# Kernel optimization log

Hardware: AMD Instinct MI355X
Metric: run time of the kernel (lower is better)

The kernel has to match this reference:

```python
import jax, jax.numpy as jnp
import numpy as np

N_USERS = 50000
N_ITEMS = 10000
N_ENTITIES = 40000
N_NODES = N_USERS + N_ITEMS + N_ENTITIES  # 100000
EMB = 64
NNZ = 1600000  # avg degree 16
VIS_DIM = 2048
TXT_DIM = 300


def setup_inputs() -> dict:
    key = jax.random.key(0)
    ks = jax.random.split(key, 16)
    def xn(k, shape, scale=0.05):
        return jax.random.normal(k, shape, dtype=jnp.float32) * scale
    return {
        "adj_row": jax.random.randint(ks[0], (NNZ,), 0, N_NODES, dtype=jnp.int32),
        "adj_col": jax.random.randint(ks[1], (NNZ,), 0, N_NODES, dtype=jnp.int32),
        "adj_val": jax.random.uniform(ks[2], (NNZ,), dtype=jnp.float32) / 16.0,  # ~normalized adj
        "embedding": xn(ks[3], (N_NODES, EMB), 0.1),
        "visual_features": jax.random.normal(ks[4], (N_ITEMS, VIS_DIM), dtype=jnp.float32),
        "text_features": jax.random.normal(ks[5], (N_ITEMS, TXT_DIM), dtype=jnp.float32),
        "Wv1": xn(ks[6], (512, VIS_DIM)), "bv1": jnp.zeros((512,), jnp.float32),
        "Wv2": xn(ks[7], (EMB, 512)),    "bv2": jnp.zeros((EMB,), jnp.float32),
        "Wt1": xn(ks[8], (256, TXT_DIM)), "bt1": jnp.zeros((256,), jnp.float32),
        "Wt2": xn(ks[9], (EMB, 256)),    "bt2": jnp.zeros((EMB,), jnp.float32),
        "Wd": xn(ks[10], (EMB, EMB)),    "bd": jnp.zeros((EMB,), jnp.float32),
        "Wc0": xn(ks[11], (EMB, 2 * EMB)), "bc0": jnp.zeros((EMB,), jnp.float32),
        "Wc1": xn(ks[12], (EMB, 2 * EMB)), "bc1": jnp.zeros((EMB,), jnp.float32),
    }


def _lin(x, W, b):
    return x @ W.T + b


def reference(adj_row, adj_col, adj_val, embedding, visual_features, text_features,
              Wv1, bv1, Wv2, bv2, Wt1, bt1, Wt2, bt2, Wd, bd, Wc0, bc0, Wc1, bc1):
    # multimodal item encoding (eval mode: dropout = identity)
    vis = _lin(jax.nn.relu(_lin(visual_features, Wv1, bv1)), Wv2, bv2)
    vis = _lin(vis, Wd, bd)
    txt = _lin(jax.nn.relu(_lin(text_features, Wt1, bt1)), Wt2, bt2)
    txt = _lin(txt, Wd, bd)
    fused_item = (vis + txt) * 0.5  # [n_items, emb]

    ego = embedding.at[N_USERS:N_USERS + N_ITEMS].set(fused_item)

    all_embs = [ego]
    cur = ego
    for Wc, bc in ((Wc0, bc0), (Wc1, bc1)):
        # SpMM: neighbor[i] = sum_j A[i,j] * cur[j]
        msgs = adj_val[:, None] * cur[adj_col]            # [nnz, emb]
        nb = jax.ops.segment_sum(msgs, adj_row, num_segments=N_NODES)
        cur = _lin(jnp.concatenate([cur, nb], axis=-1), Wc, bc)  # W_concat
        cur = jax.nn.leaky_relu(cur, 0.01)                # F.leaky_relu default slope
        all_embs.append(cur)

    return jnp.concatenate(all_embs, axis=-1)  # [n_nodes, emb*(n_layers+1)]
```

## Files before the change

kernel.cpp:

```cpp
#include <hip/hip_runtime.h>
#include <hip/hip_bf16.h>
#include <cstddef>

#define N_USERS 50000
#define N_ITEMS 10000
#define N_NODES 100000
#define EMB 64
#define NNZ_E 1600000
#define VIS_DIM 2048
#define TXT_DIM 300

typedef short bf16x8 __attribute__((ext_vector_type(8)));
typedef float f32x4  __attribute__((ext_vector_type(4)));

__device__ inline unsigned short f2bf(float x) {
    __hip_bfloat16 h = __float2bfloat16(x);
    return __builtin_bit_cast(unsigned short, h);
}
__device__ inline float bf2f(unsigned short u) {
    unsigned int t = ((unsigned int)u) << 16;
    float f;
    __builtin_memcpy(&f, &t, 4);
    return f;
}

#define GLDW 40

__global__ __launch_bounds__(256, 2) void gemm_bf64(
    const float* __restrict__ A, const float* __restrict__ W,
    const float* __restrict__ bias, float* __restrict__ C,
    int M, int N, int K, int k_per, long long c_plane,
    int act, int add_bias, int n_tiles, int m_tiles, int zsplit)
{
    __shared__ unsigned short Ah[128][GLDW], Al[128][GLDW];
    __shared__ unsigned short Bh[64][GLDW],  Bl[64][GLDW];

    const int wg     = blockIdx.x;
    const int xcd    = wg & 7;
    const int rest   = wg >> 3;
    const int nzc    = n_tiles * zsplit;
    const int nz     = rest % nzc;
    const int mchunk = rest / nzc;
    const int mt     = xcd + (mchunk << 3);
    if (mt >= m_tiles) return;
    const int nt     = nz % n_tiles;
    const int kz     = nz / n_tiles;

    const int t   = threadIdx.x;
    const int w   = t >> 6;
    const int l   = t & 63;
    const int l16 = l & 15;
    const int lq  = l >> 4;
    const int n0  = nt * 64;
    const int m0  = mt * 128;
    const int mh  = w * 32;

    const int kb  = kz * k_per;
    int krem = K - kb; if (krem > k_per) krem = k_per;
    const int kiters = (krem + 31) / 32;
    const int kend = kb + krem;
    float* Cz = C + (long long)kz * c_plane;

    const int rA0 = t >> 2;
    const int rA1 = (t + 256) >> 2;
    const int kc  = t & 3;

    f32x4 acc[2][4] = {};
    float pa[2][8], pw[8];

    auto load_tile = [&](int kt) {
        const int k0 = kb + kt * 32 + kc * 8;
        #pragma unroll
        for (int p = 0; p < 2; p++) {
            int rg = m0 + (p ? rA1 : rA0);
            if (rg >= M) rg = M - 1;
            const float* g = A + (size_t)rg * K + k0;
            if (k0 + 7 < kend) {
                float4 q0 = *(const float4*)g, q1 = *(const float4*)(g + 4);
                pa[p][0]=q0.x; pa[p][1]=q0.y; pa[p][2]=q0.z; pa[p][3]=q0.w;
                pa[p][4]=q1.x; pa[p][5]=q1.y; pa[p][6]=q1.z; pa[p][7]=q1.w;
            } else {
                #pragma unroll
                for (int i = 0; i < 8; i++)
                    pa[p][i] = (k0 + i < kend) ? g[i] : 0.f;
            }
        }
        int ng = n0 + rA0;
        if (ng >= N) ng = N - 1;
        const float* gw = W + (size_t)ng * K + k0;
        if (k0 + 7 < kend) {
            float4 q0 = *(const float4*)gw, q1 = *(const float4*)(gw + 4);
            pw[0]=q0.x; pw[1]=q0.y; pw[2]=q0.z; pw[3]=q0.w;
            pw[4]=q1.x; pw[5]=q1.y; pw[6]=q1.z; pw[7]=q1.w;
        } else {
            #pragma unroll
            for (int i = 0; i < 8; i++)
                pw[i] = (k0 + i < kend) ? gw[i] : 0.f;
        }
    };

    load_tile(0);

    for (int kt = 0; kt < kiters; kt++) {
        #pragma unroll
        for (int p = 0; p < 2; p++) {
            int row = p ? rA1 : rA0;
            bf16x8 hi, lo;
            #pragma unroll
            for (int i = 0; i < 8; i++) {
                unsigned short h = f2bf(pa[p][i]);
                hi[i] = (short)h;
                lo[i] = (short)f2bf(pa[p][i] - bf2f(h));
            }
            *(bf16x8*)&Ah[row][kc * 8] = hi;
            *(bf16x8*)&Al[row][kc * 8] = lo;
        }
        {
            bf16x8 hi, lo;
            #pragma unroll
            for (int i = 0; i < 8; i++) {
                unsigned short h = f2bf(pw[i]);
                hi[i] = (short)h;
                lo[i] = (short)f2bf(pw[i] - bf2f(h));
            }
            *(bf16x8*)&Bh[rA0][kc * 8] = hi;
            *(bf16x8*)&Bl[rA0][kc * 8] = lo;
        }
        __syncthreads();

        if (kt + 1 < kiters) load_tile(kt + 1);

        {
            bf16x8 ah[2], al[2];
            #pragma unroll
            for (int mi = 0; mi < 2; mi++) {
                ah[mi] = *(const bf16x8*)&Ah[mh + mi * 16 + l16][lq * 8];
                al[mi] = *(const bf16x8*)&Al[mh + mi * 16 + l16][lq * 8];
            }
            #pragma unroll
            for (int ni = 0; ni < 4; ni++) {
                bf16x8 bh = *(const bf16x8*)&Bh[ni * 16 + l16][lq * 8];
                bf16x8 bl = *(const bf16x8*)&Bl[ni * 16 + l16][lq * 8];
                #pragma unroll
                for (int mi = 0; mi < 2; mi++) {
                    acc[mi][ni] = __builtin_amdgcn_mfma_f32_16x16x32_bf16(
                        ah[mi], bh, acc[mi][ni], 0, 0, 0);
                    acc[mi][ni] = __builtin_amdgcn_mfma_f32_16x16x32_bf16(
                        ah[mi], bl, acc[mi][ni], 0, 0, 0);
                    acc[mi][ni] = __builtin_amdgcn_mfma_f32_16x16x32_bf16(
                        al[mi], bh, acc[mi][ni], 0, 0, 0);
                }
            }
        }
        __syncthreads();
    }

    #pragma unroll
    for (int ni = 0; ni < 4; ni++) {
        int col = n0 + ni * 16 + l16;
        if (col >= N) continue;
        float b = (add_bias && kz == 0) ? bias[col] : 0.f;
        #pragma unroll
        for (int mi = 0; mi < 2; mi++) {
            #pragma unroll
            for (int r = 0; r < 4; r++) {
                int row = m0 + mh + mi * 16 + lq * 4 + r;
                if (row >= M) continue;
                float v = acc[mi][ni][r] + b;
                if (act) v = fmaxf(v, 0.f);
                Cz[(size_t)row * N + col] = v;
            }
        }
    }
}

__global__ __launch_bounds__(256, 2) void concat_mfma(
    const float* __restrict__ cur, const float* __restrict__ nbuf,
    const float* __restrict__ Wc, const float* __restrict__ bias,
    float* __restrict__ out_cur, float* __restrict__ out_full, int col_off)
{
    __shared__ unsigned short Ah[128][GLDW], Al[128][GLDW];
    __shared__ unsigned short Bh[64][GLDW],  Bl[64][GLDW];

    const int t   = threadIdx.x;
    const int w   = t >> 6;
    const int l   = t & 63;
    const int l16 = l & 15;
    const int lq  = l >> 4;
    const int m0  = blockIdx.x * 128;
    const int mh  = w * 32;

    const int r  = t >> 2;
    const int kc = t & 3;

    f32x4 acc[2][4] = {};

    float pa[2][8], pw[8];

    auto load_tile = [&](int kt) {
        const float* src = (kt < 2) ? cur : nbuf;
        const int kcol = (kt & 1) * 32 + kc * 8;
        #pragma unroll
        for (int p = 0; p < 2; p++) {
            int rg = m0 + r + p * 64;
            if (rg >= N_NODES) rg = N_NODES - 1;
            const float* g = src + (size_t)rg * 64 + kcol;
            float4 q0 = *(const float4*)g, q1 = *(const float4*)(g + 4);
            pa[p][0]=q0.x; pa[p][1]=q0.y; pa[p][2]=q0.z; pa[p][3]=q0.w;
            pa[p][4]=q1.x; pa[p][5]=q1.y; pa[p][6]=q1.z; pa[p][7]=q1.w;
        }
        const float* gw = Wc + (size_t)r * 128 + kt * 32 + kc * 8;
        float4 q0 = *(const float4*)gw, q1 = *(const float4*)(gw + 4);
        pw[0]=q0.x; pw[1]=q0.y; pw[2]=q0.z; pw[3]=q0.w;
        pw[4]=q1.x; pw[5]=q1.y; pw[6]=q1.z; pw[7]=q1.w;
    };

    load_tile(0);

    for (int kt = 0; kt < 4; kt++) {
        #pragma unroll
        for (int p = 0; p < 2; p++) {
            bf16x8 hi, lo;
            #pragma unroll
            for (int i = 0; i < 8; i++) {
                unsigned short h = f2bf(pa[p][i]);
                hi[i] = (short)h;
                lo[i] = (short)f2bf(pa[p][i] - bf2f(h));
            }
            *(bf16x8*)&Ah[r + p * 64][kc * 8] = hi;
            *(bf16x8*)&Al[r + p * 64][kc * 8] = lo;
        }
        {
            bf16x8 hi, lo;
            #pragma unroll
            for (int i = 0; i < 8; i++) {
                unsigned short h = f2bf(pw[i]);
                hi[i] = (short)h;
                lo[i] = (short)f2bf(pw[i] - bf2f(h));
            }
            *(bf16x8*)&Bh[r][kc * 8] = hi;
            *(bf16x8*)&Bl[r][kc * 8] = lo;
        }
        __syncthreads();

        if (kt < 3) load_tile(kt + 1);

        {
            bf16x8 ah[2], al[2];
            #pragma unroll
            for (int mi = 0; mi < 2; mi++) {
                ah[mi] = *(const bf16x8*)&Ah[mh + mi * 16 + l16][lq * 8];
                al[mi] = *(const bf16x8*)&Al[mh + mi * 16 + l16][lq * 8];
            }
            #pragma unroll
            for (int ni = 0; ni < 4; ni++) {
                bf16x8 bh = *(const bf16x8*)&Bh[ni * 16 + l16][lq * 8];
                bf16x8 bl = *(const bf16x8*)&Bl[ni * 16 + l16][lq * 8];
                #pragma unroll
                for (int mi = 0; mi < 2; mi++) {
                    acc[mi][ni] = __builtin_amdgcn_mfma_f32_16x16x32_bf16(
                        ah[mi], bh, acc[mi][ni], 0, 0, 0);
                    acc[mi][ni] = __builtin_amdgcn_mfma_f32_16x16x32_bf16(
                        ah[mi], bl, acc[mi][ni], 0, 0, 0);
                    acc[mi][ni] = __builtin_amdgcn_mfma_f32_16x16x32_bf16(
                        al[mi], bh, acc[mi][ni], 0, 0, 0);
                }
            }
        }
        __syncthreads();
    }

    #pragma unroll
    for (int ni = 0; ni < 4; ni++) {
        int col = ni * 16 + l16;
        float bcol = bias[col];
        #pragma unroll
        for (int mi = 0; mi < 2; mi++) {
            #pragma unroll
            for (int rr = 0; rr < 4; rr++) {
                int row = m0 + mh + mi * 16 + lq * 4 + rr;
                if (row >= N_NODES) continue;
                float v = acc[mi][ni][rr] + bcol;
                v = (v > 0.f) ? v : 0.01f * v;
                if (out_cur) out_cur[(size_t)row * 64 + col] = v;
                out_full[(size_t)row * 192 + col_off + col] = v;
            }
        }
    }
}

__global__ void transp64(const float* __restrict__ W, float* __restrict__ wT, int K)
{
    int i = blockIdx.x * 256 + threadIdx.x;
    if (i >= 64 * K) return;
    int d = i / K, k = i - d * K;
    wT[k * 64 + d] = W[i];
}

__global__ __launch_bounds__(256) void linear64(
    const float* __restrict__ in, const float* __restrict__ in2,
    const float* __restrict__ wT, const float* __restrict__ bias,
    float* __restrict__ out, int M, int K, float in_scale, int add,
    int fuse_relu)
{
    int t  = threadIdx.x;
    int d  = t & 63;
    int w  = t >> 6;
    int m0 = blockIdx.x * 16 + w * 4;
    if (m0 >= M) return;
    int mlast = M - 1;
    int m1 = (m0 + 1 < M) ? m0 + 1 : mlast;
    int m2 = (m0 + 2 < M) ? m0 + 2 : mlast;
    int m3 = (m0 + 3 < M) ? m0 + 3 : mlast;

    const float* x0 = in + (size_t)m0 * K;
    const float* x1 = in + (size_t)m1 * K;
    const float* x2 = in + (size_t)m2 * K;
    const float* x3 = in + (size_t)m3 * K;
    const float* y0 = fuse_relu ? in2 + (size_t)m0 * K : x0;
    const float* y1 = fuse_relu ? in2 + (size_t)m1 * K : x1;
    const float* y2 = fuse_relu ? in2 + (size_t)m2 * K : x2;
    const float* y3 = fuse_relu ? in2 + (size_t)m3 * K : x3;

    float a0 = 0.f, a1 = 0.f, a2 = 0.f, a3 = 0.f;

    for (int k = 0; k < K; k += 8) {
        const float* wp = wT + (size_t)k * 64 + d;
        float w0 = wp[0],   w1 = wp[64],  w2 = wp[128], w3 = wp[192];
        float w4 = wp[256], w5 = wp[320], w6 = wp[384], w7 = wp[448];
        float4 p0 = *(const float4*)(x0 + k), q0 = *(const float4*)(x0 + k + 4);
        float4 p1 = *(const float4*)(x1 + k), q1 = *(const float4*)(x1 + k + 4);
        float4 p2 = *(const float4*)(x2 + k), q2 = *(const float4*)(x2 + k + 4);
        float4 p3 = *(const float4*)(x3 + k), q3 = *(const float4*)(x3 + k + 4);
        if (fuse_relu) {
            float4 r0 = *(const float4*)(y0 + k), s0 = *(const float4*)(y0 + k + 4);
            float4 r1 = *(const float4*)(y1 + k), s1 = *(const float4*)(y1 + k + 4);
            float4 r2 = *(const float4*)(y2 + k), s2 = *(const float4*)(y2 + k + 4);
            float4 r3 = *(const float4*)(y3 + k), s3 = *(const float4*)(y3 + k + 4);
            p0.x=fmaxf(p0.x+r0.x,0.f); p0.y=fmaxf(p0.y+r0.y,0.f);
            p0.z=fmaxf(p0.z+r0.z,0.f); p0.w=fmaxf(p0.w+r0.w,0.f);
            q0.x=fmaxf(q0.x+s0.x,0.f); q0.y=fmaxf(q0.y+s0.y,0.f);
            q0.z=fmaxf(q0.z+s0.z,0.f); q0.w=fmaxf(q0.w+s0.w,0.f);
            p1.x=fmaxf(p1.x+r1.x,0.f); p1.y=fmaxf(p1.y+r1.y,0.f);
            p1.z=fmaxf(p1.z+r1.z,0.f); p1.w=fmaxf(p1.w+r1.w,0.f);
            q1.x=fmaxf(q1.x+s1.x,0.f); q1.y=fmaxf(q1.y+s1.y,0.f);
            q1.z=fmaxf(q1.z+s1.z,0.f); q1.w=fmaxf(q1.w+s1.w,0.f);
            p2.x=fmaxf(p2.x+r2.x,0.f); p2.y=fmaxf(p2.y+r2.y,0.f);
            p2.z=fmaxf(p2.z+r2.z,0.f); p2.w=fmaxf(p2.w+r2.w,0.f);
            q2.x=fmaxf(q2.x+s2.x,0.f); q2.y=fmaxf(q2.y+s2.y,0.f);
            q2.z=fmaxf(q2.z+s2.z,0.f); q2.w=fmaxf(q2.w+s2.w,0.f);
            p3.x=fmaxf(p3.x+r3.x,0.f); p3.y=fmaxf(p3.y+r3.y,0.f);
            p3.z=fmaxf(p3.z+r3.z,0.f); p3.w=fmaxf(p3.w+r3.w,0.f);
            q3.x=fmaxf(q3.x+s3.x,0.f); q3.y=fmaxf(q3.y+s3.y,0.f);
            q3.z=fmaxf(q3.z+s3.z,0.f); q3.w=fmaxf(q3.w+s3.w,0.f);
        }
        a0 += p0.x*w0 + p0.y*w1 + p0.z*w2 + p0.w*w3
            + q0.x*w4 + q0.y*w5 + q0.z*w6 + q0.w*w7;
        a1 += p1.x*w0 + p1.y*w1 + p1.z*w2 + p1.w*w3
            + q1.x*w4 + q1.y*w5 + q1.z*w6 + q1.w*w7;
        a2 += p2.x*w0 + p2.y*w1 + p2.z*w2 + p2.w*w3
            + q2.x*w4 + q2.y*w5 + q2.z*w6 + q2.w*w7;
        a3 += p3.x*w0 + p3.y*w1 + p3.z*w2 + p3.w*w3
            + q3.x*w4 + q3.y*w5 + q3.z*w6 + q3.w*w7;
    }

    float b = bias[d];
    float r0 = a0 * in_scale + b;
    float r1 = a1 * in_scale + b;
    float r2 = a2 * in_scale + b;
    float r3 = a3 * in_scale + b;
    if (add) {
        out[(size_t)m0 * 64 + d] += r0;
        if (m0 + 1 < M) out[(size_t)m1 * 64 + d] += r1;
        if (m0 + 2 < M) out[(size_t)m2 * 64 + d] += r2;
        if (m0 + 3 < M) out[(size_t)m3 * 64 + d] += r3;
    } else {
        out[(size_t)m0 * 64 + d] = r0;
        if (m0 + 1 < M) out[(size_t)m1 * 64 + d] = r1;
        if (m0 + 2 < M) out[(size_t)m2 * 64 + d] = r2;
        if (m0 + 3 < M) out[(size_t)m3 * 64 + d] = r3;
    }
}

__global__ void ego_fill(const float* __restrict__ emb, float* __restrict__ cur0,
                         float* __restrict__ out_full)
{
    int tid = blockIdx.x * 256 + threadIdx.x;
    if (tid >= N_NODES * EMB) return;
    int m = tid >> 6, d = tid & 63;
    float v;
    if (m < N_USERS || m >= N_USERS + N_ITEMS) {
        v = emb[tid];
        cur0[tid] = v;
    } else {
        v = cur0[tid];
    }
    out_full[(size_t)m * 192 + d] = v;
}

__global__ __launch_bounds__(256) void hist_rows(
    const int* __restrict__ row, int* __restrict__ cnt, int nnz)
{
    int e = blockIdx.x * 256 + threadIdx.x;
    if (e >= nnz) return;
    atomicAdd(&cnt[row[e]], 1);
}

__global__ __launch_bounds__(256) void scan1(int* __restrict__ cnt,
                                             int* __restrict__ bsum, int n)
{
    __shared__ int part[256];
    int t = threadIdx.x;
    int base = blockIdx.x * 1024 + t * 4;
    int v0 = 0, v1 = 0, v2 = 0, v3 = 0;
    if (base + 0 < n) v0 = cnt[base + 0];
    if (base + 1 < n) v1 = cnt[base + 1];
    if (base + 2 < n) v2 = cnt[base + 2];
    if (base + 3 < n) v3 = cnt[base + 3];
    int s = v0 + v1 + v2 + v3;
    part[t] = s;
    __syncthreads();
    for (int off = 1; off < 256; off <<= 1) {
        int x = (t >= off) ? part[t - off] : 0;
        __syncthreads();
        part[t] += x;
        __syncthreads();
    }
    int excl = part[t] - s;
    if (t == 255) bsum[blockIdx.x] = part[t];
    if (base + 0 < n) cnt[base + 0] = excl;
    if (base + 1 < n) cnt[base + 1] = excl + v0;
    if (base + 2 < n) cnt[base + 2] = excl + v0 + v1;
    if (base + 3 < n) cnt[base + 3] = excl + v0 + v1 + v2;
}

__global__ void scan2(int* __restrict__ bsum, int nb)
{
    if (threadIdx.x == 0 && blockIdx.x == 0) {
        int acc = 0;
        for (int i = 0; i < nb; i++) { int v = bsum[i]; bsum[i] = acc; acc += v; }
    }
}

__global__ __launch_bounds__(256) void scan3(
    const int* __restrict__ excl, const int* __restrict__ bsum,
    int* __restrict__ row_ptr, int* __restrict__ row_cur, int n, int nnz)
{
    int i = blockIdx.x * 256 + threadIdx.x;
    if (i > n) return;
    if (i == n) { row_ptr[n] = nnz; return; }
    int v = excl[i] + bsum[i >> 10];
    row_ptr[i] = v;
    row_cur[i] = v;
}

__global__ __launch_bounds__(256) void scatter_csr(
    const int* __restrict__ row, const int* __restrict__ col,
    const float* __restrict__ val, int* __restrict__ row_cur,
    int* __restrict__ col_s, float* __restrict__ val_s, int nnz)
{
    int e = blockIdx.x * 256 + threadIdx.x;
    if (e >= nnz) return;
    int r = row[e];
    int p = atomicAdd(&row_cur[r], 1);
    col_s[p] = col[e];
    val_s[p] = val[e];
}

__global__ __launch_bounds__(256) void spmm_gather(
    const int* __restrict__ row_ptr, const int* __restrict__ col_s,
    const float* __restrict__ val_s, const float* __restrict__ cur,
    float* __restrict__ nb)
{
    int t  = threadIdx.x;
    int wv = t >> 6;
    int l  = t & 63;
    int eg = l >> 4;
    int dg = l & 15;
    int m = blockIdx.x * 4 + wv;
    if (m >= N_NODES) return;
    int beg = row_ptr[m], end = row_ptr[m + 1];
    float ax = 0.f, ay = 0.f, az = 0.f, aw = 0.f;
    for (int j = beg + eg; j < end; j += 4) {
        int   c = col_s[j];
        float v = val_s[j];
        float4 cv = *(const float4*)&cur[(size_t)c * 64 + dg * 4];
        ax += v * cv.x; ay += v * cv.y; az += v * cv.z; aw += v * cv.w;
    }
    ax += __shfl_xor(ax, 16, 64); ay += __shfl_xor(ay, 16, 64);
    az += __shfl_xor(az, 16, 64); aw += __shfl_xor(aw, 16, 64);
    ax += __shfl_xor(ax, 32, 64); ay += __shfl_xor(ay, 32, 64);
    az += __shfl_xor(az, 32, 64); aw += __shfl_xor(aw, 32, 64);
    if (eg == 0) {
        float4 r; r.x = ax; r.y = ay; r.z = az; r.w = aw;
        *(float4*)&nb[(size_t)m * 64 + dg * 4] = r;
    }
}

extern "C" void kernel_launch(void* const* d_in, const int* in_sizes, int n_in,
                              void* d_out, int out_size, void* d_ws, size_t ws_size,
                              hipStream_t stream)
{
    const int*   adj_row = (const int*)  d_in[0];
    const int*   adj_col = (const int*)  d_in[1];
    const float* adj_val = (const float*)d_in[2];
    const float* emb     = (const float*)d_in[3];
    const float* visf    = (const float*)d_in[4];
    const float* txtf    = (const float*)d_in[5];
    const float* Wv1 = (const float*)d_in[6];  const float* bv1 = (const float*)d_in[7];
    const float* Wv2 = (const float*)d_in[8];  const float* bv2 = (const float*)d_in[9];
    const float* Wt1 = (const float*)d_in[10]; const float* bt1 = (const float*)d_in[11];
    const float* Wt2 = (const float*)d_in[12]; const float* bt2 = (const float*)d_in[13];
    const float* Wd  = (const float*)d_in[14]; const float* bd  = (const float*)d_in[15];
    const float* Wc0 = (const float*)d_in[16]; const float* bc0 = (const float*)d_in[17];
    const float* Wc1 = (const float*)d_in[18]; const float* bc1 = (const float*)d_in[19];

    float* out = (float*)d_out;
    float* ws  = (float*)d_ws;

    float* H1v  = ws + 0;
    float* H1t  = ws + 5120000;
    float* nb   = ws + 0;
    float* s    = ws + 7680000;
    float* cur0 = ws + 8320000;
    float* cur1 = ws + 14720000;
    float* H1v2 = ws + 14720000;
    float* wv2T = ws + 21120000;
    float* wt2T = wv2T + 32768;
    float* wdT  = wt2T + 16384;
    int*   col_s   = (int*)  (ws + 21200000);
    float* val_s   =          ws + 22800000;
    int*   row_ptr = (int*)  (ws + 24400000);
    int*   row_cur = (int*)  (ws + 24510000);
    int*   cnt     = (int*)  (ws + 24620000);
    int*   bsum    = (int*)  (ws + 24730000);

    const int NBLK = (N_NODES + 1023) / 1024;

    transp64<<<(64 * 512 + 255) / 256, 256, 0, stream>>>(Wv2, wv2T, 512);
    transp64<<<(64 * 256 + 255) / 256, 256, 0, stream>>>(Wt2, wt2T, 256);
    transp64<<<(64 * 64  + 255) / 256, 256, 0, stream>>>(Wd,  wdT,  64);

    hipMemsetAsync(cnt, 0, N_NODES * sizeof(int), stream);
    hist_rows<<<(NNZ_E + 255) / 256, 256, 0, stream>>>(adj_row, cnt, NNZ_E);
    scan1<<<NBLK, 256, 0, stream>>>(cnt, bsum, N_NODES);
    scan2<<<1, 64, 0, stream>>>(bsum, NBLK);
    scan3<<<(N_NODES + 256) / 256, 256, 0, stream>>>(cnt, bsum, row_ptr, row_cur,
                                                     N_NODES, NNZ_E);
    scatter_csr<<<(NNZ_E + 255) / 256, 256, 0, stream>>>(adj_row, adj_col, adj_val,
                                                         row_cur, col_s, val_s, NNZ_E);

    {
        int n_tiles = 8, m_tiles = 79, zsplit = 2;
        int grid = 8 * n_tiles * zsplit * ((m_tiles + 7) / 8);
        gemm_bf64<<<grid, 256, 0, stream>>>(visf, Wv1, bv1, H1v,
                                            N_ITEMS, 512, VIS_DIM,
                                            1024, (long long)14720000, 0, 1,
                                            n_tiles, m_tiles, zsplit);
    }
    {
        int n_tiles = 4, m_tiles = 79, zsplit = 1;
        int grid = 8 * n_tiles * zsplit * ((m_tiles + 7) / 8);
        gemm_bf64<<<grid, 256, 0, stream>>>(txtf, Wt1, bt1, H1t,
                                            N_ITEMS, 256, TXT_DIM,
                                            512, 0, 1, 1,
                                            n_tiles, m_tiles, zsplit);
    }

    linear64<<<(N_ITEMS + 15) / 16, 256, 0, stream>>>(H1v, H1v2, wv2T, bv2, s,
                                                      N_ITEMS, 512, 1.0f, 0, 1);
    linear64<<<(N_ITEMS + 15) / 16, 256, 0, stream>>>(H1t, nullptr, wt2T, bt2, s,
                                                      N_ITEMS, 256, 1.0f, 1, 0);
    linear64<<<(N_ITEMS + 15) / 16, 256, 0, stream>>>(s, nullptr, wdT, bd,
                                                      cur0 + (size_t)N_USERS * 64,
                                                      N_ITEMS, 64, 0.5f, 0, 0);

    ego_fill<<<(N_NODES * EMB + 255) / 256, 256, 0, stream>>>(emb, cur0, out);

    spmm_gather<<<(N_NODES + 3) / 4, 256, 0, stream>>>(row_ptr, col_s, val_s, cur0, nb);
    concat_mfma<<<(N_NODES + 127) / 128, 256, 0, stream>>>(cur0, nb, Wc0, bc0, cur1, out, 64);

    spmm_gather<<<(N_NODES + 3) / 4, 256, 0, stream>>>(row_ptr, col_s, val_s, cur1, nb);
    concat_mfma<<<(N_NODES + 127) / 128, 256, 0, stream>>>(cur1, nb, Wc1, bc1, nullptr, out, 128);
}
```

Before: 819.2 us.

## Pre-split weights into bf16 hi/lo MFMA fragments and load B from global

Adds a prepass kernel that splits each weight matrix into bf16 high/low parts, stored in an MFMA-fragment-tiled layout. The GEMM and concat kernels then read B fragments directly from global/L2 instead of converting per tile and staging through LDS. This removes the repeated weight splitting and the B shared-memory traffic, and raises the occupancy hint to 4 blocks. In exchange it adds extra launches and puts uncoalesced-ish global loads on the critical path of the MFMA loop.

```diff
diff --git a/kernel.cpp b/kernel.cpp
--- a/kernel.cpp
+++ b/kernel.cpp
@@ -26,14 +26,37 @@
 
 #define GLDW 40
 
-__global__ __launch_bounds__(256, 2) void gemm_bf64(
-    const float* __restrict__ A, const float* __restrict__ W,
+__global__ __launch_bounds__(256) void wsplit_frag(
+    const float* __restrict__ W, unsigned short* __restrict__ Wh,
+    unsigned short* __restrict__ Wl, int N, int K, int Kp)
+{
+    int idx = blockIdx.x * 256 + threadIdx.x;
+    int ncell = Kp >> 3;
+    if (idx >= N * ncell) return;
+    int n = idx / ncell, kcell = idx - n * ncell;
+    int k0 = kcell * 8;
+    bf16x8 hi, lo;
+    #pragma unroll
+    for (int i = 0; i < 8; i++) {
+        float v = (k0 + i < K) ? W[(size_t)n * K + k0 + i] : 0.f;
+        unsigned short h = f2bf(v);
+        hi[i] = (short)h;
+        lo[i] = (short)f2bf(v - bf2f(h));
+    }
+    size_t off = ((size_t)(n >> 4) * ncell + kcell) * 128 + (size_t)(n & 15) * 8;
+    *(bf16x8*)(Wh + off) = hi;
+    *(bf16x8*)(Wl + off) = lo;
+}
+
+__global__ __launch_bounds__(256, 4) void gemm_bf64(
+    const float* __restrict__ A,
+    const unsigned short* __restrict__ Wh_f,
+    const unsigned short* __restrict__ Wl_f,
     const float* __restrict__ bias, float* __restrict__ C,
-    int M, int N, int K, int k_per, long long c_plane,
+    int M, int N, int K, int Kp, int k_per, long long c_plane,
     int act, int add_bias, int n_tiles, int m_tiles, int zsplit)
 {
     __shared__ unsigned short Ah[128][GLDW], Al[128][GLDW];
-    __shared__ unsigned short Bh[64][GLDW],  Bl[64][GLDW];
 
     const int wg     = blockIdx.x;
     const int xcd    = wg & 7;
@@ -61,14 +84,16 @@
     const int kend = kb + krem;
     float* Cz = C + (long long)kz * c_plane;
 
+    const int ncell = Kp >> 3;
+
     const int rA0 = t >> 2;
     const int rA1 = (t + 256) >> 2;
     const int kc  = t & 3;
 
     f32x4 acc[2][4] = {};
-    float pa[2][8], pw[8];
-
-    auto load_tile = [&](int kt) {
+    float pa[2][8];
+
+    auto load_tileA = [&](int kt) {
         const int k0 = kb + kt * 32 + kc * 8;
         #pragma unroll
         for (int p = 0; p < 2; p++) {
@@ -85,21 +110,9 @@
                     pa[p][i] = (k0 + i < kend) ? g[i] : 0.f;
             }
         }
-        int ng = n0 + rA0;
-        if (ng >= N) ng = N - 1;
-        const float* gw = W + (size_t)ng * K + k0;
-        if (k0 + 7 < kend) {
-            float4 q0 = *(const float4*)gw, q1 = *(const float4*)(gw + 4);
-            pw[0]=q0.x; pw[1]=q0.y; pw[2]=q0.z; pw[3]=q0.w;
-            pw[4]=q1.x; pw[5]=q1.y; pw[6]=q1.z; pw[7]=q1.w;
-        } else {
-            #pragma unroll
-            for (int i = 0; i < 8; i++)
-                pw[i] = (k0 + i < kend) ? gw[i] : 0.f;
-        }
     };
 
-    load_tile(0);
+    load_tileA(0);
 
     for (int kt = 0; kt < kiters; kt++) {
         #pragma unroll
@@ -115,20 +128,21 @@
             *(bf16x8*)&Ah[row][kc * 8] = hi;
             *(bf16x8*)&Al[row][kc * 8] = lo;
         }
+        __syncthreads();
+
+        bf16x8 bh[4], bl[4];
         {
-            bf16x8 hi, lo;
-            #pragma unroll
-            for (int i = 0; i < 8; i++) {
-                unsigned short h = f2bf(pw[i]);
-                hi[i] = (short)h;
-                lo[i] = (short)f2bf(pw[i] - bf2f(h));
-            }
-            *(bf16x8*)&Bh[rA0][kc * 8] = hi;
-            *(bf16x8*)&Bl[rA0][kc * 8] = lo;
-        }
-        __syncthreads();
-
-        if (kt + 1 < kiters) load_tile(kt + 1);
+            const int kch = ((kb + kt * 32) >> 3) + lq;
+            #pragma unroll
+            for (int ni = 0; ni < 4; ni++) {
+                size_t off = ((size_t)((n0 >> 4) + ni) * ncell + kch) * 128
+                           + (size_t)l16 * 8;
+                bh[ni] = *(const bf16x8*)(Wh_f + off);
+                bl[ni] = *(const bf16x8*)(Wl_f + off);
+            }
+        }
+
+        if (kt + 1 < kiters) load_tileA(kt + 1);
 
         {
             bf16x8 ah[2], al[2];
@@ -139,16 +153,14 @@
             }
             #pragma unroll
             for (int ni = 0; ni < 4; ni++) {
-                bf16x8 bh = *(const bf16x8*)&Bh[ni * 16 + l16][lq * 8];
-                bf16x8 bl = *(const bf16x8*)&Bl[ni * 16 + l16][lq * 8];
                 #pragma unroll
                 for (int mi = 0; mi < 2; mi++) {
                     acc[mi][ni] = __builtin_amdgcn_mfma_f32_16x16x32_bf16(
-                        ah[mi], bh, acc[mi][ni], 0, 0, 0);
+                        ah[mi], bh[ni], acc[mi][ni], 0, 0, 0);
                     acc[mi][ni] = __builtin_amdgcn_mfma_f32_16x16x32_bf16(
-                        ah[mi], bl, acc[mi][ni], 0, 0, 0);
+                        ah[mi], bl[ni], acc[mi][ni], 0, 0, 0);
                     acc[mi][ni] = __builtin_amdgcn_mfma_f32_16x16x32_bf16(
-                        al[mi], bh, acc[mi][ni], 0, 0, 0);
+                        al[mi], bh[ni], acc[mi][ni], 0, 0, 0);
                 }
             }
         }
@@ -174,13 +186,14 @@
     }
 }
 
-__global__ __launch_bounds__(256, 2) void concat_mfma(
+__global__ __launch_bounds__(256, 4) void concat_mfma(
     const float* __restrict__ cur, const float* __restrict__ nbuf,
-    const float* __restrict__ Wc, const float* __restrict__ bias,
+    const unsigned short* __restrict__ Wch,
+    const unsigned short* __restrict__ Wcl,
+    const float* __restrict__ bias,
     float* __restrict__ out_cur, float* __restrict__ out_full, int col_off)
 {
     __shared__ unsigned short Ah[128][GLDW], Al[128][GLDW];
-    __shared__ unsigned short Bh[64][GLDW],  Bl[64][GLDW];
 
     const int t   = threadIdx.x;
     const int w   = t >> 6;
@@ -194,10 +207,9 @@
     const int kc = t & 3;
 
     f32x4 acc[2][4] = {};
-
-    float pa[2][8], pw[8];
-
-    auto load_tile = [&](int kt) {
+    float pa[2][8];
+
+    auto load_tileA = [&](int kt) {
         const float* src = (kt < 2) ? cur : nbuf;
         const int kcol = (kt & 1) * 32 + kc * 8;
         #pragma unroll
@@ -209,13 +221,9 @@
             pa[p][0]=q0.x; pa[p][1]=q0.y; pa[p][2]=q0.z; pa[p][3]=q0.w;
             pa[p][4]=q1.x; pa[p][5]=q1.y; pa[p][6]=q1.z; pa[p][7]=q1.w;
         }
-        const float* gw = Wc + (size_t)r * 128 + kt * 32 + kc * 8;
-        float4 q0 = *(const float4*)gw, q1 = *(const float4*)(gw + 4);
-        pw[0]=q0.x; pw[1]=q0.y; pw[2]=q0.z; pw[3]=q0.w;
-        pw[4]=q1.x; pw[5]=q1.y; pw[6]=q1.z; pw[7]=q1.w;
     };
 
-    load_tile(0);
+    load_tileA(0);
 
     for (int kt = 0; kt < 4; kt++) {
         #pragma unroll
@@ -230,20 +238,20 @@
             *(bf16x8*)&Ah[r + p * 64][kc * 8] = hi;
             *(bf16x8*)&Al[r + p * 64][kc * 8] = lo;
         }
+        __syncthreads();
+
+        bf16x8 bh[4], bl[4];
         {
-            bf16x8 hi, lo;
-            #pragma unroll
-            for (int i = 0; i < 8; i++) {
-                unsigned short h = f2bf(pw[i]);
-                hi[i] = (short)h;
-                lo[i] = (short)f2bf(pw[i] - bf2f(h));
-            }
-            *(bf16x8*)&Bh[r][kc * 8] = hi;
-            *(bf16x8*)&Bl[r][kc * 8] = lo;
-        }
-        __syncthreads();
-
-        if (kt < 3) load_tile(kt + 1);
+            const int kch = (kt * 32 >> 3) + lq;
+            #pragma unroll
+            for (int ni = 0; ni < 4; ni++) {
+                size_t off = ((size_t)ni * 16 + kch) * 128 + (size_t)l16 * 8;
+                bh[ni] = *(const bf16x8*)(Wch + off);
+                bl[ni] = *(const bf16x8*)(Wcl + off);
+            }
+        }
+
+        if (kt < 3) load_tileA(kt + 1);
 
         {
             bf16x8 ah[2], al[2];
@@ -254,16 +262,14 @@
             }
             #pragma unroll
             for (int ni = 0; ni < 4; ni++) {
-                bf16x8 bh = *(const bf16x8*)&Bh[ni * 16 + l16][lq * 8];
-                bf16x8 bl = *(const bf16x8*)&Bl[ni * 16 + l16][lq * 8];
                 #pragma unroll
                 for (int mi = 0; mi < 2; mi++) {
                     acc[mi][ni] = __builtin_amdgcn_mfma_f32_16x16x32_bf16(
-                        ah[mi], bh, acc[mi][ni], 0, 0, 0);
+                        ah[mi], bh[ni], acc[mi][ni], 0, 0, 0);
                     acc[mi][ni] = __builtin_amdgcn_mfma_f32_16x16x32_bf16(
-                        ah[mi], bl, acc[mi][ni], 0, 0, 0);
+                        ah[mi], bl[ni], acc[mi][ni], 0, 0, 0);
                     acc[mi][ni] = __builtin_amdgcn_mfma_f32_16x16x32_bf16(
-                        al[mi], bh, acc[mi][ni], 0, 0, 0);
+                        al[mi], bh[ni], acc[mi][ni], 0, 0, 0);
                 }
             }
         }
@@ -528,6 +534,16 @@
     float* wv2T = ws + 21120000;
     float* wt2T = wv2T + 32768;
     float* wdT  = wt2T + 16384;
+
+    unsigned short* Wv1h = (unsigned short*)(ws + 5120000);
+    unsigned short* Wv1l = (unsigned short*)(ws + 5644288);
+    unsigned short* Wt1h = (unsigned short*)(ws + 7680000);
+    unsigned short* Wt1l = (unsigned short*)(ws + 7720960);
+    unsigned short* Wc0h = (unsigned short*)(ws + 21173248);
+    unsigned short* Wc0l = (unsigned short*)(ws + 21177344);
+    unsigned short* Wc1h = (unsigned short*)(ws + 21181440);
+    unsigned short* Wc1l = (unsigned short*)(ws + 21185536);
+
     int*   col_s   = (int*)  (ws + 21200000);
     float* val_s   =          ws + 22800000;
     int*   row_ptr = (int*)  (ws + 24400000);
@@ -540,6 +556,14 @@
     transp64<<<(64 * 512 + 255) / 256, 256, 0, stream>>>(Wv2, wv2T, 512);
     transp64<<<(64 * 256 + 255) / 256, 256, 0, stream>>>(Wt2, wt2T, 256);
     transp64<<<(64 * 64  + 255) / 256, 256, 0, stream>>>(Wd,  wdT,  64);
+    wsplit_frag<<<(512 * 256 + 255) / 256, 256, 0, stream>>>(Wv1, Wv1h, Wv1l,
+                                                             512, 2048, 2048);
+    wsplit_frag<<<(256 * 40 + 255) / 256, 256, 0, stream>>>(Wt1, Wt1h, Wt1l,
+                                                            256, 300, 320);
+    wsplit_frag<<<(64 * 16 + 255) / 256, 256, 0, stream>>>(Wc0, Wc0h, Wc0l,
+                                                           64, 128, 128);
+    wsplit_frag<<<(64 * 16 + 255) / 256, 256, 0, stream>>>(Wc1, Wc1h, Wc1l,
+                                                           64, 128, 128);
 
     hipMemsetAsync(cnt, 0, N_NODES * sizeof(int), stream);
     hist_rows<<<(NNZ_E + 255) / 256, 256, 0, stream>>>(adj_row, cnt, NNZ_E);
@@ -553,16 +577,16 @@
     {
         int n_tiles = 8, m_tiles = 79, zsplit = 2;
         int grid = 8 * n_tiles * zsplit * ((m_tiles + 7) / 8);
-        gemm_bf64<<<grid, 256, 0, stream>>>(visf, Wv1, bv1, H1v,
-                                            N_ITEMS, 512, VIS_DIM,
+        gemm_bf64<<<grid, 256, 0, stream>>>(visf, Wv1h, Wv1l, bv1, H1v,
+                                            N_ITEMS, 512, VIS_DIM, 2048,
                                             1024, (long long)14720000, 0, 1,
                                             n_tiles, m_tiles, zsplit);
     }
     {
         int n_tiles = 4, m_tiles = 79, zsplit = 1;
         int grid = 8 * n_tiles * zsplit * ((m_tiles + 7) / 8);
-        gemm_bf64<<<grid, 256, 0, stream>>>(txtf, Wt1, bt1, H1t,
-                                            N_ITEMS, 256, TXT_DIM,
+        gemm_bf64<<<grid, 256, 0, stream>>>(txtf, Wt1h, Wt1l, bt1, H1t,
+                                            N_ITEMS, 256, TXT_DIM, 320,
                                             512, 0, 1, 1,
                                             n_tiles, m_tiles, zsplit);
     }
@@ -578,8 +602,10 @@
     ego_fill<<<(N_NODES * EMB + 255) / 256, 256, 0, stream>>>(emb, cur0, out);
 
     spmm_gather<<<(N_NODES + 3) / 4, 256, 0, stream>>>(row_ptr, col_s, val_s, cur0, nb);
-    concat_mfma<<<(N_NODES + 127) / 128, 256, 0, stream>>>(cur0, nb, Wc0, bc0, cur1, out, 64);
+    concat_mfma<<<(N_NODES + 127) / 128, 256, 0, stream>>>(cur0, nb, Wc0h, Wc0l, bc0,
+                                                           cur1, out, 64);
 
     spmm_gather<<<(N_NODES + 3) / 4, 256, 0, stream>>>(row_ptr, col_s, val_s, cur1, nb);
-    concat_mfma<<<(N_NODES + 127) / 128, 256, 0, stream>>>(cur1, nb, Wc1, bc1, nullptr, out, 128);
-}
+    concat_mfma<<<(N_NODES + 127) / 128, 256, 0, stream>>>(cur1, nb, Wc1h, Wc1l, bc1,
+                                                           nullptr, out, 128);
+}
```

Result: slower. 853.4 us (+4.2%).
